# Optimization experiments

Measured on AMD Instinct MI355X. Metric: run time of the kernel, lower is better.

Reference implementation:

```python
import jax, jax.numpy as jnp
import numpy as np


def relu_bt(x):
    # -threshold(-leaky_relu(x), -t, -t) == min(leaky_relu(x), t), t = ||x||_inf (detached)
    t = jax.lax.stop_gradient(jnp.max(jnp.abs(x)))
    return jnp.minimum(jax.nn.leaky_relu(x, negative_slope=0.01), t)


def setup_inputs() -> dict:
    key = jax.random.key(0)
    k1, k2, k3, k4 = jax.random.split(key, 4)
    N, E, F_in, F_out = 100000, 1600000, 128, 64
    x = jax.random.normal(k1, (N, F_in), dtype=jnp.float32)
    edge_index = jax.random.randint(k2, (2, E), 0, N, dtype=jnp.int64)
    # xavier_normal with gain=1.414
    W = jax.random.normal(k3, (F_in, F_out), dtype=jnp.float32) * (1.414 * np.sqrt(2.0 / (F_in + F_out)))
    a = jax.random.normal(k4, (1, 4 * F_out), dtype=jnp.float32) * (1.414 * np.sqrt(2.0 / (1 + 4 * F_out)))
    return {"x": x, "edge_index": edge_index, "W": W, "a": a}


def reference(x, edge_index, W, a):
    N = x.shape[0]
    F_out = W.shape[1]
    h = x @ W  # [N, F_out]
    src = edge_index[0]
    dst = edge_index[1]
    hs = h[src]  # [E, F_out]
    hd = h[dst]  # [E, F_out]
    agg = relu_bt(hs + hd)
    diff = relu_bt(hs - hd)
    # a @ cat([hs, hd, agg, diff], dim=1).T == sum of four per-edge dot products
    a0, a1, a2, a3 = jnp.split(a.reshape(4 * F_out), 4)
    score = hs @ a0 + hd @ a1 + agg @ a2 + diff @ a3  # [E]
    edge_e = jnp.exp(-relu_bt(score))  # [E]
    # spmm(A, ones): rowsum over outgoing edges (grouped by src)
    e_rowsum = jax.ops.segment_sum(edge_e, src, num_segments=N)  # [N]
    # spmm(A, h): weighted aggregation of neighbor (dst) features into src rows
    h_prime = jax.ops.segment_sum(edge_e[:, None] * hd, src, num_segments=N)  # [N, F_out]
    return h_prime / (e_rowsum[:, None] + 1e-16)
```

## Files before the change

### kernel.cpp

```cpp
#include <hip/hip_runtime.h>
#include <hip/hip_fp16.h>

#define F_IN 128
#define F_OUT 64
#define BIN_TILE 2048
#define BSHIFT 8
#define BNODES 256
#define BCAP 6144u

#define LK_A 0.505f
#define LK_B 0.495f

__device__ __forceinline__ float leaky(float v) {
    return fmaf(LK_B, fabsf(v), LK_A * v);
}

template <int CTRL>
__device__ __forceinline__ float dppadd(float v) {
    return v + __builtin_bit_cast(float,
        __builtin_amdgcn_update_dpp(0, __builtin_bit_cast(int, v), CTRL, 0xf, 0xf, true));
}

__device__ __forceinline__ float sum8(float v) {
    v = dppadd<0xB1>(v);
    v = dppadd<0x4E>(v);
    v = dppadd<0x141>(v);
    return v;
}

__device__ __forceinline__ float xslot_sum2(float v) {
    v = dppadd<0x128>(v);
    v += __shfl_xor(v, 16);
    return v;
}

__device__ __forceinline__ float wave_sum(float v) {
    v += __builtin_bit_cast(float, __builtin_amdgcn_update_dpp(0, __builtin_bit_cast(int, v), 0x111, 0xf, 0xf, true));
    v += __builtin_bit_cast(float, __builtin_amdgcn_update_dpp(0, __builtin_bit_cast(int, v), 0x112, 0xf, 0xf, true));
    v += __builtin_bit_cast(float, __builtin_amdgcn_update_dpp(0, __builtin_bit_cast(int, v), 0x114, 0xf, 0xe, true));
    v += __builtin_bit_cast(float, __builtin_amdgcn_update_dpp(0, __builtin_bit_cast(int, v), 0x118, 0xf, 0xc, true));
    v += __builtin_bit_cast(float, __builtin_amdgcn_update_dpp(0, __builtin_bit_cast(int, v), 0x142, 0xa, 0xf, true));
    v += __builtin_bit_cast(float, __builtin_amdgcn_update_dpp(0, __builtin_bit_cast(int, v), 0x143, 0xc, 0xf, true));
    return __builtin_bit_cast(float, __builtin_amdgcn_readlane(__builtin_bit_cast(int, v), 63));
}

__device__ __forceinline__ void cvt8(const uint4 u, float* g) {
    float2 f;
    f = __half22float2(__builtin_bit_cast(__half2, u.x)); g[0] = f.x; g[1] = f.y;
    f = __half22float2(__builtin_bit_cast(__half2, u.y)); g[2] = f.x; g[3] = f.y;
    f = __half22float2(__builtin_bit_cast(__half2, u.z)); g[4] = f.x; g[5] = f.y;
    f = __half22float2(__builtin_bit_cast(__half2, u.w)); g[6] = f.x; g[7] = f.y;
}

__global__ __launch_bounds__(256) void gemm_xw(const float* __restrict__ x,
                                               const float* __restrict__ W,
                                               float* __restrict__ h32,
                                               uint2* __restrict__ h16,
                                               unsigned* __restrict__ gcur,
                                               int N, int NB, unsigned cap, int mode) {
    if (gcur && blockIdx.x == 0)
        for (int i = threadIdx.x; i < NB; i += 256) gcur[i] = (unsigned)i * cap;

    __shared__ float w_lds[F_IN][F_OUT];
    {
        const float4* Wv = (const float4*)W;
        float4* wl = (float4*)w_lds;
        for (int i = threadIdx.x; i < F_IN * F_OUT / 4; i += 256) wl[i] = Wv[i];
    }
    __syncthreads();

    const int cg = threadIdx.x & 15;
    const int rs = threadIdx.x >> 4;
    const int row0 = blockIdx.x * 128 + rs * 8;

    int r[8];
#pragma unroll
    for (int i = 0; i < 8; ++i) { const int rr = row0 + i; r[i] = rr < N ? rr : N - 1; }

    float4 acc[8];
#pragma unroll
    for (int i = 0; i < 8; ++i) acc[i] = make_float4(0.f, 0.f, 0.f, 0.f);

    float4 xc[8];
#pragma unroll
    for (int i = 0; i < 8; ++i) xc[i] = *(const float4*)(x + (size_t)r[i] * F_IN);

    for (int k4 = 0; k4 < 32; ++k4) {
        float4 xn[8];
        if (k4 < 31) {
#pragma unroll
            for (int i = 0; i < 8; ++i)
                xn[i] = *(const float4*)(x + (size_t)r[i] * F_IN + (k4 + 1) * 4);
        }
        float4 wv[4];
#pragma unroll
        for (int kk = 0; kk < 4; ++kk)
            wv[kk] = *(const float4*)&w_lds[k4 * 4 + kk][cg * 4];

#pragma unroll
        for (int i = 0; i < 8; ++i) {
            acc[i].x = fmaf(xc[i].x, wv[0].x, acc[i].x);
            acc[i].y = fmaf(xc[i].x, wv[0].y, acc[i].y);
            acc[i].z = fmaf(xc[i].x, wv[0].z, acc[i].z);
            acc[i].w = fmaf(xc[i].x, wv[0].w, acc[i].w);
            acc[i].x = fmaf(xc[i].y, wv[1].x, acc[i].x);
            acc[i].y = fmaf(xc[i].y, wv[1].y, acc[i].y);
            acc[i].z = fmaf(xc[i].y, wv[1].z, acc[i].z);
            acc[i].w = fmaf(xc[i].y, wv[1].w, acc[i].w);
            acc[i].x = fmaf(xc[i].z, wv[2].x, acc[i].x);
            acc[i].y = fmaf(xc[i].z, wv[2].y, acc[i].y);
            acc[i].z = fmaf(xc[i].z, wv[2].z, acc[i].z);
            acc[i].w = fmaf(xc[i].z, wv[2].w, acc[i].w);
            acc[i].x = fmaf(xc[i].w, wv[3].x, acc[i].x);
            acc[i].y = fmaf(xc[i].w, wv[3].y, acc[i].y);
            acc[i].z = fmaf(xc[i].w, wv[3].z, acc[i].z);
            acc[i].w = fmaf(xc[i].w, wv[3].w, acc[i].w);
        }
        if (k4 < 31) {
#pragma unroll
            for (int i = 0; i < 8; ++i) xc[i] = xn[i];
        }
    }

#pragma unroll
    for (int i = 0; i < 8; ++i) {
        const int rr = row0 + i;
        if (rr < N) {
            if (mode & 2) *(float4*)(h32 + (size_t)rr * F_OUT + cg * 4) = acc[i];
            if (mode & 1) {
                uint2 u;
                u.x = __builtin_bit_cast(unsigned, __floats2half2_rn(acc[i].x, acc[i].y));
                u.y = __builtin_bit_cast(unsigned, __floats2half2_rn(acc[i].z, acc[i].w));
                h16[(size_t)rr * 16 + cg] = u;
            }
        }
    }
}

__global__ __launch_bounds__(256) void binA(const int* __restrict__ ei,
                                            unsigned* __restrict__ gcur,
                                            unsigned* __restrict__ binned,
                                            int E, int NB, unsigned cap) {
    __shared__ unsigned lcnt[1024];
    __shared__ unsigned lbase[1024];
    const int t = threadIdx.x;
    for (int i = t; i < NB; i += 256) lcnt[i] = 0;
    __syncthreads();
    const int base = blockIdx.x * BIN_TILE;
    unsigned pk[8], bk[8], rk[8];
#pragma unroll
    for (int i = 0; i < 8; ++i) {
        const int e = base + i * 256 + t;
        if (e < E) {
            const unsigned s = (unsigned)ei[e];
            const unsigned d = (unsigned)ei[E + e];
            bk[i] = s >> BSHIFT;
            pk[i] = ((s & (BNODES - 1u)) << 17) | d;
            rk[i] = atomicAdd(&lcnt[bk[i]], 1u);
        }
    }
    __syncthreads();
    for (int i = t; i < NB; i += 256) {
        const unsigned c = lcnt[i];
        lbase[i] = c ? atomicAdd(&gcur[i], c) : 0u;
    }
    __syncthreads();
#pragma unroll
    for (int i = 0; i < 8; ++i) {
        const int e = base + i * 256 + t;
        if (e < E) {
            const unsigned pos = lbase[bk[i]] + rk[i];
            if (pos < (bk[i] + 1u) * cap) binned[pos] = pk[i];
        }
    }
}

__global__ __launch_bounds__(256) void binB(const unsigned* __restrict__ binned,
                                            const unsigned* __restrict__ gcur,
                                            unsigned* __restrict__ off,
                                            unsigned* __restrict__ deg,
                                            int* __restrict__ sdst,
                                            int N, int NB, unsigned cap) {
    __shared__ unsigned stg[BCAP];
    __shared__ unsigned ncnt[BNODES];
    __shared__ unsigned ts[256];
    const int b = blockIdx.x;
    const int t = threadIdx.x;
    const unsigned src0 = (unsigned)b * cap;
    unsigned sz = gcur[b] - src0; if (sz > cap) sz = cap;

    ncnt[t] = 0;
    for (unsigned i = t; i < sz; i += 256) stg[i] = binned[src0 + i];
    __syncthreads();

    for (unsigned i = t; i < sz; i += 256) atomicAdd(&ncnt[stg[i] >> 17], 1u);
    __syncthreads();

    const unsigned myc = ncnt[t];
    ts[t] = myc;
    __syncthreads();
    for (int st = 1; st < 256; st <<= 1) {
        const unsigned add = (t >= st) ? ts[t - st] : 0u;
        __syncthreads();
        ts[t] += add;
        __syncthreads();
    }
    const unsigned excl = ts[t] - myc;
    ncnt[t] = excl;
    const int g = (b << BSHIFT) + t;
    if (g < N) { off[g] = src0 + excl; deg[g] = myc; }
    __syncthreads();

    for (unsigned i = t; i < sz; i += 256) {
        const unsigned p = stg[i];
        const unsigned pos = atomicAdd(&ncnt[p >> 17], 1u);
        sdst[src0 + pos] = (int)(p & 0x1FFFFu);
    }
}

__global__ __launch_bounds__(256) void node_kernel(const unsigned* __restrict__ off,
                                                   const unsigned* __restrict__ deg,
                                                   const int* __restrict__ sdst,
                                                   const uint2* __restrict__ h16v,
                                                   const float* __restrict__ a,
                                                   float* __restrict__ out, int N) {
    const int lane  = threadIdx.x & 63;
    const int half  = lane >> 5;
    const int slot4 = (lane >> 3) & 3;
    const int q     = lane & 7;
    const char* h16 = (const char*)h16v;

    float b1[8], a2b[8], a3b[8], a0m[8];
#pragma unroll
    for (int f = 0; f < 8; ++f) {
        const float A0 = a[q * 8 + f];
        const float A1 = a[64 + q * 8 + f];
        const float A2 = a[128 + q * 8 + f];
        const float A3 = a[192 + q * 8 + f];
        b1[f]  = fmaf(LK_A, A2 - A3, A1);
        a2b[f] = LK_B * A2;
        a3b[f] = LK_B * A3;
        a0m[f] = fmaf(LK_A, A2 + A3, A0);
    }

    const int wid = (int)((blockIdx.x * 256u + threadIdx.x) >> 6);
    const int nw  = (int)((gridDim.x * 256u) >> 6);

    int pr = wid;
    if (pr * 2 >= N) return;

    int node = pr * 2 + half;
    int nc = (node < N) ? node : N - 1;
    unsigned bg  = off[nc];
    unsigned dgv = (node < N) ? deg[nc] : 0u;
    uint4 hsu = *(const uint4*)(h16 + ((size_t)nc << 7) + q * 16);
    int dA0 = 0;
    {
        const int len0 = (int)dgv;
        if (len0 > 0) { int e0 = slot4; const int lm = len0 - 1; if (e0 > lm) e0 = lm; dA0 = sdst[bg + e0]; }
    }

    while (true) {
        const int prn = pr + nw;
        const bool hasNext = (prn * 2 < N);

        const int len = (int)dgv;
        const unsigned beg = bg;
        float hs[8]; cvt8(hsu, hs);

        int noden = 0, ncn = 0; unsigned bgn = 0, dgn = 0;
        uint4 hsun = make_uint4(0u, 0u, 0u, 0u);
        if (hasNext) {
            noden = prn * 2 + half;
            ncn = (noden < N) ? noden : N - 1;
            bgn = off[ncn];
            dgn = (noden < N) ? deg[ncn] : 0u;
            hsun = *(const uint4*)(h16 + ((size_t)ncn << 7) + q * 16);
        }

        float csp = 0.f;
#pragma unroll
        for (int f = 0; f < 8; ++f) csp = fmaf(hs[f], a0m[f], csp);
        const float cs = sum8(csp);

        const int lenO = __shfl_xor(len, 32);
        const int ml = (len > lenO) ? len : lenO;

        float acc[8];
#pragma unroll
        for (int f = 0; f < 8; ++f) acc[f] = 0.f;
        float rsum = 0.f;

        const int lm1 = (len > 0) ? len - 1 : 0;
        uint4 uA = *(const uint4*)(h16 + ((size_t)dA0 << 7) + q * 16);
        int dB = dA0;
        if (len > 4) { int e1 = 4 + slot4; if (e1 > lm1) e1 = lm1; dB = sdst[beg + e1]; }
        uint4 uB = *(const uint4*)(h16 + ((size_t)dB << 7) + q * 16);
        int dC = dB;
        if (len > 8) { int e2 = 8 + slot4; if (e2 > lm1) e2 = lm1; dC = sdst[beg + e2]; }

        for (int cb = 0; cb < ml; cb += 4) {
            uint4 uC = uB;
            int dD = dC;
            if (cb + 8 < len)
                uC = *(const uint4*)(h16 + ((size_t)dC << 7) + q * 16);
            if (cb + 12 < len) { int e3 = cb + 12 + slot4; if (e3 > lm1) e3 = lm1; dD = sdst[beg + e3]; }

            float g[8];
            cvt8(uA, g);
            float p0 = 0.f, p1 = 0.f;
#pragma unroll
            for (int f = 0; f < 8; f += 2) {
                const float sa0 = hs[f] + g[f],         sb0 = hs[f] - g[f];
                const float sa1 = hs[f + 1] + g[f + 1], sb1 = hs[f + 1] - g[f + 1];
                p0 = fmaf(g[f],     b1[f],     p0);
                p1 = fmaf(g[f + 1], b1[f + 1], p1);
                p0 = fmaf(fabsf(sa0), a2b[f],     p0);
                p1 = fmaf(fabsf(sa1), a2b[f + 1], p1);
                p0 = fmaf(fabsf(sb0), a3b[f],     p0);
                p1 = fmaf(fabsf(sb1), a3b[f + 1], p1);
            }
            const float R = sum8(p0 + p1);

            float e = __expf(-leaky(cs + R));
            e = (cb + slot4 < len) ? e : 0.f;
#pragma unroll
            for (int f = 0; f < 8; ++f) acc[f] = fmaf(e, g[f], acc[f]);
            rsum += e;

            uA = uB; uB = uC; dC = dD;
        }

        int dA0n = 0;
        if (hasNext) {
            const int lenn = (int)dgn;
            if (lenn > 0) { int e0 = slot4; const int lm = lenn - 1; if (e0 > lm) e0 = lm; dA0n = sdst[bgn + e0]; }
        }

#pragma unroll
        for (int f = 0; f < 8; ++f) acc[f] = xslot_sum2(acc[f]);
        rsum = xslot_sum2(rsum);

        if (slot4 == 0 && node < N) {
            const float inv = 1.f / (rsum + 1e-16f);
            float4 o0, o1;
            o0.x = acc[0] * inv; o0.y = acc[1] * inv; o0.z = acc[2] * inv; o0.w = acc[3] * inv;
            o1.x = acc[4] * inv; o1.y = acc[5] * inv; o1.z = acc[6] * inv; o1.w = acc[7] * inv;
            float* orow = out + (size_t)node * F_OUT + q * 8;
            *(float4*)orow = o0;
            *(float4*)(orow + 4) = o1;
        }

        if (!hasNext) break;
        pr = prn; node = noden; nc = ncn; bg = bgn; dgv = dgn; hsu = hsun; dA0 = dA0n;
    }
}

__global__ __launch_bounds__(256) void hist_kernel(const int* __restrict__ ei,
                                                   unsigned* __restrict__ cnt, int E) {
    const int e = blockIdx.x * 256 + threadIdx.x;
    if (e < E) atomicAdd(&cnt[ei[e]], 1u);
}

__global__ __launch_bounds__(256) void scan1(const unsigned* __restrict__ cnt,
                                             unsigned* __restrict__ bsum, int n) {
    __shared__ unsigned lds[256];
    const int t = threadIdx.x;
    const int base = blockIdx.x * 2048 + t * 8;
    unsigned s = 0;
#pragma unroll
    for (int i = 0; i < 8; ++i) { const int idx = base + i; if (idx < n) s += cnt[idx]; }
    lds[t] = s; __syncthreads();
    for (int st = 128; st > 0; st >>= 1) {
        if (t < st) lds[t] += lds[t + st];
        __syncthreads();
    }
    if (t == 0) bsum[blockIdx.x] = lds[0];
}

__global__ __launch_bounds__(128) void scan2(unsigned* __restrict__ bsum,
                                             unsigned* __restrict__ off, int nb, int n) {
    __shared__ unsigned lds[128];
    const int t = threadIdx.x;
    if (t < nb) lds[t] = bsum[t];
    __syncthreads();
    if (t == 0) {
        unsigned run = 0;
        for (int i = 0; i < nb; ++i) { const unsigned v = lds[i]; lds[i] = run; run += v; }
        off[n] = run;
    }
    __syncthreads();
    if (t < nb) bsum[t] = lds[t];
}

__global__ __launch_bounds__(256) void scan3(const unsigned* __restrict__ cnt,
                                             const unsigned* __restrict__ bsum,
                                             unsigned* __restrict__ off,
                                             unsigned* __restrict__ cursor, int n) {
    __shared__ unsigned lds[256];
    const int t = threadIdx.x;
    const int base = blockIdx.x * 2048 + t * 8;
    unsigned v[8]; unsigned s = 0;
#pragma unroll
    for (int i = 0; i < 8; ++i) { const int idx = base + i; v[i] = (idx < n) ? cnt[idx] : 0u; s += v[i]; }
    lds[t] = s; __syncthreads();
    for (int st = 1; st < 256; st <<= 1) {
        const unsigned add = (t >= st) ? lds[t - st] : 0u;
        __syncthreads();
        lds[t] += add;
        __syncthreads();
    }
    unsigned excl = (t > 0 ? lds[t - 1] : 0u) + bsum[blockIdx.x];
#pragma unroll
    for (int i = 0; i < 8; ++i) {
        const int idx = base + i;
        if (idx < n) { off[idx] = excl; cursor[idx] = excl; excl += v[i]; }
    }
}

__global__ __launch_bounds__(256) void scatter_kernel(const int* __restrict__ ei,
                                                      unsigned* __restrict__ cursor,
                                                      int* __restrict__ sdst, int E) {
    const int e = blockIdx.x * 256 + threadIdx.x;
    if (e >= E) return;
    const int s = ei[e];
    const int d = ei[E + e];
    const unsigned pos = atomicAdd(&cursor[s], 1u);
    sdst[pos] = d;
}

__device__ __forceinline__ float edge_part(float hs, float hd, float a1, float a2, float a3) {
    float p = hd * a1;
    p = fmaf(leaky(hs + hd), a2, p);
    p = fmaf(leaky(hs - hd), a3, p);
    return p;
}

__global__ __launch_bounds__(256) void edge_kernel(const int* __restrict__ ei,
                                                   const float* __restrict__ h,
                                                   const float* __restrict__ a,
                                                   float* __restrict__ hprime,
                                                   float* __restrict__ rowsum,
                                                   int E) {
    const int lane = threadIdx.x & 63;
    const int wave = (int)((blockIdx.x * blockDim.x + threadIdx.x) >> 6);
    const int nwaves = (int)((gridDim.x * blockDim.x) >> 6);
    const float a0 = a[lane], a1 = a[64 + lane], a2 = a[128 + lane], a3 = a[192 + lane];
    for (int e = wave; e < E; e += nwaves) {
        const int s = ei[e];
        const int d = ei[E + e];
        const float hs = h[(size_t)s * F_OUT + lane];
        const float hd = h[(size_t)d * F_OUT + lane];
        const float part = wave_sum(hs * a0 + edge_part(hs, hd, a1, a2, a3));
        const float ee = __expf(-leaky(part));
        atomicAdd(&hprime[(size_t)s * F_OUT + lane], ee * hd);
        if (lane == 0) atomicAdd(&rowsum[s], ee);
    }
}

__global__ __launch_bounds__(256) void finalize(float* __restrict__ out,
                                                const float* __restrict__ rowsum,
                                                int total) {
    const int i = blockIdx.x * blockDim.x + threadIdx.x;
    if (i < total) out[i] = out[i] / (rowsum[i >> 6] + 1e-16f);
}

static inline size_t align_up(size_t v, size_t a) { return (v + a - 1) & ~(a - 1); }

extern "C" void kernel_launch(void* const* d_in, const int* in_sizes, int n_in,
                              void* d_out, int out_size, void* d_ws, size_t ws_size,
                              hipStream_t stream) {
    const float* x  = (const float*)d_in[0];
    const int*   ei = (const int*)d_in[1];
    const float* W  = (const float*)d_in[2];
    const float* a  = (const float*)d_in[3];

    const int N = in_sizes[0] / F_IN;
    const int E = in_sizes[1] / 2;
    float* out = (float*)d_out;

    const int NB = (N + BNODES - 1) >> BSHIFT;
    const int ngemm = (N + 127) / 128;
    const int nbt = (E + BIN_TILE - 1) / BIN_TILE;
    const unsigned meanFill = (NB > 0) ? (unsigned)(E / NB) : 0u;

    char* ws = (char*)d_ws;
    const size_t szh16  = align_up((size_t)N * F_OUT * 2, 256);
    const size_t szoff  = align_up(((size_t)N + 1) * 4, 256);
    const size_t szedge = align_up((size_t)E * 4 + 64, 256);
    const size_t szbin  = align_up((size_t)NB * BCAP * 4 + 64, 256);

    const size_t off_b  = szh16;
    const size_t deg_b    = off_b + szoff;
    const size_t sdstA_b  = deg_b + szoff;
    const size_t binned_b = sdstA_b + szbin;
    const size_t gcur_b   = binned_b + szbin;
    const size_t needA    = gcur_b + 4096;
    const size_t sdstB_b  = off_b + szoff;
    const size_t cursor_b = sdstB_b + szedge;
    const size_t cnt_b    = cursor_b + align_up((size_t)N * 4, 256);
    const size_t bsum_b   = cnt_b + align_up((size_t)N * 4, 256);
    const size_t needB    = bsum_b + 4096;

    uint2* h16 = (uint2*)ws;
    const int nodeBlocks = 2048;

    if (ws_size >= needA && N <= (1 << 17) && NB <= 1024 && meanFill <= (BCAP * 3u) / 4u) {
        unsigned* off    = (unsigned*)(ws + off_b);
        unsigned* deg    = (unsigned*)(ws + deg_b);
        int*      sdst   = (int*)(ws + sdstA_b);
        unsigned* binned = (unsigned*)(ws + binned_b);
        unsigned* gcur   = (unsigned*)(ws + gcur_b);

        gemm_xw<<<ngemm, 256, 0, stream>>>(x, W, nullptr, h16, gcur, N, NB, BCAP, 1);
        binA<<<nbt, 256, 0, stream>>>(ei, gcur, binned, E, NB, BCAP);
        binB<<<NB, 256, 0, stream>>>(binned, gcur, off, deg, sdst, N, NB, BCAP);
        node_kernel<<<nodeBlocks, 256, 0, stream>>>(off, deg, sdst, h16, a, out, N);
    } else if (ws_size >= needB && N <= (1 << 17)) {
        unsigned* off    = (unsigned*)(ws + off_b);
        int*      sdst   = (int*)(ws + sdstB_b);
        unsigned* cursor = (unsigned*)(ws + cursor_b);
        unsigned* cnt    = (unsigned*)(ws + cnt_b);
        unsigned* bsum   = (unsigned*)(ws + bsum_b);
        const int nb2 = (N + 2047) / 2048;

        hipMemsetAsync(cnt, 0, (size_t)N * 4, stream);
        gemm_xw<<<ngemm, 256, 0, stream>>>(x, W, nullptr, h16, nullptr, N, NB, BCAP, 1);
        hist_kernel<<<(E + 255) / 256, 256, 0, stream>>>(ei, cnt, E);
        scan1<<<nb2, 256, 0, stream>>>(cnt, bsum, N);
        scan2<<<1, 128, 0, stream>>>(bsum, off, nb2, N);
        scan3<<<nb2, 256, 0, stream>>>(cnt, bsum, off, cursor, N);
        scatter_kernel<<<(E + 255) / 256, 256, 0, stream>>>(ei, cursor, sdst, E);
        node_kernel<<<nodeBlocks, 256, 0, stream>>>(off, cnt, sdst, h16, a, out, N);
    } else {
        float* h32    = (float*)ws;
        float* rowsum = (float*)(ws + align_up((size_t)N * F_OUT * 4, 256));
        hipMemsetAsync(d_out, 0, (size_t)N * F_OUT * sizeof(float), stream);
        hipMemsetAsync(rowsum, 0, (size_t)N * sizeof(float), stream);
        gemm_xw<<<ngemm, 256, 0, stream>>>(x, W, h32, nullptr, nullptr, N, NB, BCAP, 2);
        edge_kernel<<<2048, 256, 0, stream>>>(ei, h32, a, out, rowsum, E);
        finalize<<<((size_t)N * F_OUT + 255) / 256, 256, 0, stream>>>(out, rowsum, N * F_OUT);
    }
}
```

Baseline: 147.5 us.

## Fuse GEMM with edge binning and merge bucket sort into per-bucket node kernel

Merges the x@W GEMM and the first edge-binning pass into one launch, with blocks split by index so the two jobs run concurrently. Bins shrink to 64 nodes each, and a new bucket_node kernel does the per-node counting sort in LDS and then computes attention and aggregation straight from the staged edges. It also stages source-node features in LDS, which removes the separate binB pass and its global sdst/off/deg round trip. The cost is more, smaller bins with fixed capacity, so overflow risk rises when degree is skewed, and node work per block is tied to bucket size.

New measurement: 131.4 us. 1.12x faster.

```diff
diff --git a/kernel.cpp b/kernel.cpp
--- a/kernel.cpp
+++ b/kernel.cpp
@@ -4,9 +4,9 @@
 #define F_IN 128
 #define F_OUT 64
 #define BIN_TILE 2048
-#define BSHIFT 8
-#define BNODES 256
-#define BCAP 6144u
+#define BSHIFT 6
+#define BNODES 64
+#define BCAP 2048u
 
 #define LK_A 0.505f
 #define LK_B 0.495f
@@ -52,170 +52,354 @@
     f = __half22float2(__builtin_bit_cast(__half2, u.w)); g[6] = f.x; g[7] = f.y;
 }
 
-__global__ __launch_bounds__(256) void gemm_xw(const float* __restrict__ x,
-                                               const float* __restrict__ W,
-                                               float* __restrict__ h32,
-                                               uint2* __restrict__ h16,
-                                               unsigned* __restrict__ gcur,
-                                               int N, int NB, unsigned cap, int mode) {
-    if (gcur && blockIdx.x == 0)
-        for (int i = threadIdx.x; i < NB; i += 256) gcur[i] = (unsigned)i * cap;
-
-    __shared__ float w_lds[F_IN][F_OUT];
-    {
-        const float4* Wv = (const float4*)W;
-        float4* wl = (float4*)w_lds;
-        for (int i = threadIdx.x; i < F_IN * F_OUT / 4; i += 256) wl[i] = Wv[i];
-    }
-    __syncthreads();
-
-    const int cg = threadIdx.x & 15;
-    const int rs = threadIdx.x >> 4;
-    const int row0 = blockIdx.x * 128 + rs * 8;
-
-    int r[8];
-#pragma unroll
-    for (int i = 0; i < 8; ++i) { const int rr = row0 + i; r[i] = rr < N ? rr : N - 1; }
-
-    float4 acc[8];
-#pragma unroll
-    for (int i = 0; i < 8; ++i) acc[i] = make_float4(0.f, 0.f, 0.f, 0.f);
-
-    float4 xc[8];
-#pragma unroll
-    for (int i = 0; i < 8; ++i) xc[i] = *(const float4*)(x + (size_t)r[i] * F_IN);
-
-    for (int k4 = 0; k4 < 32; ++k4) {
-        float4 xn[8];
-        if (k4 < 31) {
-#pragma unroll
-            for (int i = 0; i < 8; ++i)
-                xn[i] = *(const float4*)(x + (size_t)r[i] * F_IN + (k4 + 1) * 4);
-        }
-        float4 wv[4];
-#pragma unroll
-        for (int kk = 0; kk < 4; ++kk)
-            wv[kk] = *(const float4*)&w_lds[k4 * 4 + kk][cg * 4];
+__global__ __launch_bounds__(256) void gemm_binA(const float* __restrict__ x,
+                                                 const float* __restrict__ W,
+                                                 float* __restrict__ h32,
+                                                 uint2* __restrict__ h16,
+                                                 const int* __restrict__ ei,
+                                                 unsigned* __restrict__ gcur,
+                                                 unsigned* __restrict__ binned,
+                                                 int N, int E, int NB, int ngemm,
+                                                 unsigned cap, int mode) {
+    __shared__ unsigned smem_u[8192];
+
+    if ((int)blockIdx.x < ngemm) {
+        float (*w_lds)[F_OUT] = (float (*)[F_OUT])smem_u;
+        {
+            const float4* Wv = (const float4*)W;
+            float4* wl = (float4*)w_lds;
+            for (int i = threadIdx.x; i < F_IN * F_OUT / 4; i += 256) wl[i] = Wv[i];
+        }
+        __syncthreads();
+
+        const int cg = threadIdx.x & 15;
+        const int rs = threadIdx.x >> 4;
+        const int row0 = blockIdx.x * 128 + rs * 8;
+
+        int r[8];
+#pragma unroll
+        for (int i = 0; i < 8; ++i) { const int rr = row0 + i; r[i] = rr < N ? rr : N - 1; }
+
+        float4 acc[8];
+#pragma unroll
+        for (int i = 0; i < 8; ++i) acc[i] = make_float4(0.f, 0.f, 0.f, 0.f);
+
+        float4 xc[8];
+#pragma unroll
+        for (int i = 0; i < 8; ++i) xc[i] = *(const float4*)(x + (size_t)r[i] * F_IN);
+
+        for (int k4 = 0; k4 < 32; ++k4) {
+            float4 xn[8];
+            if (k4 < 31) {
+#pragma unroll
+                for (int i = 0; i < 8; ++i)
+                    xn[i] = *(const float4*)(x + (size_t)r[i] * F_IN + (k4 + 1) * 4);
+            }
+            float4 wv[4];
+#pragma unroll
+            for (int kk = 0; kk < 4; ++kk)
+                wv[kk] = *(const float4*)&w_lds[k4 * 4 + kk][cg * 4];
+
+#pragma unroll
+            for (int i = 0; i < 8; ++i) {
+                acc[i].x = fmaf(xc[i].x, wv[0].x, acc[i].x);
+                acc[i].y = fmaf(xc[i].x, wv[0].y, acc[i].y);
+                acc[i].z = fmaf(xc[i].x, wv[0].z, acc[i].z);
+                acc[i].w = fmaf(xc[i].x, wv[0].w, acc[i].w);
+                acc[i].x = fmaf(xc[i].y, wv[1].x, acc[i].x);
+                acc[i].y = fmaf(xc[i].y, wv[1].y, acc[i].y);
+                acc[i].z = fmaf(xc[i].y, wv[1].z, acc[i].z);
+                acc[i].w = fmaf(xc[i].y, wv[1].w, acc[i].w);
+                acc[i].x = fmaf(xc[i].z, wv[2].x, acc[i].x);
+                acc[i].y = fmaf(xc[i].z, wv[2].y, acc[i].y);
+                acc[i].z = fmaf(xc[i].z, wv[2].z, acc[i].z);
+                acc[i].w = fmaf(xc[i].z, wv[2].w, acc[i].w);
+                acc[i].x = fmaf(xc[i].w, wv[3].x, acc[i].x);
+                acc[i].y = fmaf(xc[i].w, wv[3].y, acc[i].y);
+                acc[i].z = fmaf(xc[i].w, wv[3].z, acc[i].z);
+                acc[i].w = fmaf(xc[i].w, wv[3].w, acc[i].w);
+            }
+            if (k4 < 31) {
+#pragma unroll
+                for (int i = 0; i < 8; ++i) xc[i] = xn[i];
+            }
+        }
 
 #pragma unroll
         for (int i = 0; i < 8; ++i) {
-            acc[i].x = fmaf(xc[i].x, wv[0].x, acc[i].x);
-            acc[i].y = fmaf(xc[i].x, wv[0].y, acc[i].y);
-            acc[i].z = fmaf(xc[i].x, wv[0].z, acc[i].z);
-            acc[i].w = fmaf(xc[i].x, wv[0].w, acc[i].w);
-            acc[i].x = fmaf(xc[i].y, wv[1].x, acc[i].x);
-            acc[i].y = fmaf(xc[i].y, wv[1].y, acc[i].y);
-            acc[i].z = fmaf(xc[i].y, wv[1].z, acc[i].z);
-            acc[i].w = fmaf(xc[i].y, wv[1].w, acc[i].w);
-            acc[i].x = fmaf(xc[i].z, wv[2].x, acc[i].x);
-            acc[i].y = fmaf(xc[i].z, wv[2].y, acc[i].y);
-            acc[i].z = fmaf(xc[i].z, wv[2].z, acc[i].z);
-            acc[i].w = fmaf(xc[i].z, wv[2].w, acc[i].w);
-            acc[i].x = fmaf(xc[i].w, wv[3].x, acc[i].x);
-            acc[i].y = fmaf(xc[i].w, wv[3].y, acc[i].y);
-            acc[i].z = fmaf(xc[i].w, wv[3].z, acc[i].z);
-            acc[i].w = fmaf(xc[i].w, wv[3].w, acc[i].w);
-        }
-        if (k4 < 31) {
-#pragma unroll
-            for (int i = 0; i < 8; ++i) xc[i] = xn[i];
-        }
-    }
-
-#pragma unroll
-    for (int i = 0; i < 8; ++i) {
-        const int rr = row0 + i;
-        if (rr < N) {
-            if (mode & 2) *(float4*)(h32 + (size_t)rr * F_OUT + cg * 4) = acc[i];
-            if (mode & 1) {
-                uint2 u;
-                u.x = __builtin_bit_cast(unsigned, __floats2half2_rn(acc[i].x, acc[i].y));
-                u.y = __builtin_bit_cast(unsigned, __floats2half2_rn(acc[i].z, acc[i].w));
-                h16[(size_t)rr * 16 + cg] = u;
-            }
-        }
-    }
-}
-
-__global__ __launch_bounds__(256) void binA(const int* __restrict__ ei,
-                                            unsigned* __restrict__ gcur,
-                                            unsigned* __restrict__ binned,
-                                            int E, int NB, unsigned cap) {
-    __shared__ unsigned lcnt[1024];
-    __shared__ unsigned lbase[1024];
-    const int t = threadIdx.x;
-    for (int i = t; i < NB; i += 256) lcnt[i] = 0;
-    __syncthreads();
-    const int base = blockIdx.x * BIN_TILE;
-    unsigned pk[8], bk[8], rk[8];
-#pragma unroll
-    for (int i = 0; i < 8; ++i) {
-        const int e = base + i * 256 + t;
-        if (e < E) {
-            const unsigned s = (unsigned)ei[e];
-            const unsigned d = (unsigned)ei[E + e];
-            bk[i] = s >> BSHIFT;
-            pk[i] = ((s & (BNODES - 1u)) << 17) | d;
-            rk[i] = atomicAdd(&lcnt[bk[i]], 1u);
-        }
-    }
-    __syncthreads();
-    for (int i = t; i < NB; i += 256) {
-        const unsigned c = lcnt[i];
-        lbase[i] = c ? atomicAdd(&gcur[i], c) : 0u;
-    }
-    __syncthreads();
-#pragma unroll
-    for (int i = 0; i < 8; ++i) {
-        const int e = base + i * 256 + t;
-        if (e < E) {
-            const unsigned pos = lbase[bk[i]] + rk[i];
-            if (pos < (bk[i] + 1u) * cap) binned[pos] = pk[i];
-        }
-    }
-}
-
-__global__ __launch_bounds__(256) void binB(const unsigned* __restrict__ binned,
-                                            const unsigned* __restrict__ gcur,
-                                            unsigned* __restrict__ off,
-                                            unsigned* __restrict__ deg,
-                                            int* __restrict__ sdst,
-                                            int N, int NB, unsigned cap) {
+            const int rr = row0 + i;
+            if (rr < N) {
+                if (mode & 2) *(float4*)(h32 + (size_t)rr * F_OUT + cg * 4) = acc[i];
+                if (mode & 1) {
+                    uint2 u;
+                    u.x = __builtin_bit_cast(unsigned, __floats2half2_rn(acc[i].x, acc[i].y));
+                    u.y = __builtin_bit_cast(unsigned, __floats2half2_rn(acc[i].z, acc[i].w));
+                    h16[(size_t)rr * 16 + cg] = u;
+                }
+            }
+        }
+    } else {
+        unsigned* lcnt  = smem_u;
+        unsigned* lbase = smem_u + 2048;
+        const int t = threadIdx.x;
+        for (int i = t; i < NB; i += 256) lcnt[i] = 0;
+        __syncthreads();
+        const int base = ((int)blockIdx.x - ngemm) * BIN_TILE;
+        unsigned pk[8], bk[8], rk[8];
+#pragma unroll
+        for (int i = 0; i < 8; ++i) {
+            const int e = base + i * 256 + t;
+            if (e < E) {
+                const unsigned s = (unsigned)ei[e];
+                const unsigned d = (unsigned)ei[E + e];
+                bk[i] = s >> BSHIFT;
+                pk[i] = ((s & (BNODES - 1u)) << 17) | d;
+                rk[i] = atomicAdd(&lcnt[bk[i]], 1u);
+            }
+        }
+        __syncthreads();
+        for (int i = t; i < NB; i += 256) {
+            const unsigned c = lcnt[i];
+            lbase[i] = c ? atomicAdd(&gcur[i], c) : 0u;
+        }
+        __syncthreads();
+#pragma unroll
+        for (int i = 0; i < 8; ++i) {
+            const int e = base + i * 256 + t;
+            if (e < E) {
+                const unsigned po = lbase[bk[i]] + rk[i];
+                if (po < cap) binned[(size_t)bk[i] * cap + po] = pk[i];
+            }
+        }
+    }
+}
+
+__global__ __launch_bounds__(256) void bucket_node(const unsigned* __restrict__ binned,
+                                                   const unsigned* __restrict__ gcur,
+                                                   const uint2* __restrict__ h16v,
+                                                   const float* __restrict__ a,
+                                                   float* __restrict__ out,
+                                                   int N, unsigned cap) {
     __shared__ unsigned stg[BCAP];
-    __shared__ unsigned ncnt[BNODES];
-    __shared__ unsigned ts[256];
+    __shared__ uint4    hsl[BNODES * 8];
+    __shared__ unsigned ndeg[BNODES];
+    __shared__ unsigned nbase[BNODES];
+    __shared__ unsigned ncur[BNODES];
+    __shared__ unsigned ts[BNODES];
+
     const int b = blockIdx.x;
     const int t = threadIdx.x;
-    const unsigned src0 = (unsigned)b * cap;
-    unsigned sz = gcur[b] - src0; if (sz > cap) sz = cap;
-
-    ncnt[t] = 0;
-    for (unsigned i = t; i < sz; i += 256) stg[i] = binned[src0 + i];
+    const int node0 = b << BSHIFT;
+    const size_t src0 = (size_t)b * cap;
+    unsigned sz = gcur[b]; if (sz > cap) sz = cap;
+
+    if (t < BNODES) ndeg[t] = 0;
+    {
+        const uint4* hsrc = (const uint4*)h16v;
+        const int limit = N * 8;
+#pragma unroll
+        for (int k = 0; k < (BNODES * 8) / 256; ++k) {
+            const int i = k * 256 + t;
+            const int gi = node0 * 8 + i;
+            hsl[i] = (gi < limit) ? hsrc[gi] : make_uint4(0u, 0u, 0u, 0u);
+        }
+    }
     __syncthreads();
 
-    for (unsigned i = t; i < sz; i += 256) atomicAdd(&ncnt[stg[i] >> 17], 1u);
+    for (unsigned i = t; i < sz; i += 256)
+        atomicAdd(&ndeg[binned[src0 + i] >> 17], 1u);
     __syncthreads();
 
-    const unsigned myc = ncnt[t];
-    ts[t] = myc;
+    if (t < BNODES) ts[t] = ndeg[t];
     __syncthreads();
+    for (int st = 1; st < BNODES; st <<= 1) {
+        unsigned add = 0;
+        if (t < BNODES && t >= st) add = ts[t - st];
+        __syncthreads();
+        if (t < BNODES) ts[t] += add;
+        __syncthreads();
+    }
+    if (t < BNODES) {
+        const unsigned ex = ts[t] - ndeg[t];
+        nbase[t] = ex;
+        ncur[t]  = ex;
+    }
+    __syncthreads();
+
+    for (unsigned i = t; i < sz; i += 256) {
+        const unsigned p = binned[src0 + i];
+        const unsigned pos = atomicAdd(&ncur[p >> 17], 1u);
+        stg[pos] = p & 0x1FFFFu;
+    }
+    __syncthreads();
+
+    const int lane  = t & 63;
+    const int half  = lane >> 5;
+    const int slot4 = (lane >> 3) & 3;
+    const int q     = lane & 7;
+    const int slot8 = (t >> 6) * 2 + half;
+    const char* h16 = (const char*)h16v;
+
+    float b1[8], a2b[8], a3b[8], a0m[8];
+#pragma unroll
+    for (int f = 0; f < 8; ++f) {
+        const float A0 = a[q * 8 + f];
+        const float A1 = a[64 + q * 8 + f];
+        const float A2 = a[128 + q * 8 + f];
+        const float A3 = a[192 + q * 8 + f];
+        b1[f]  = fmaf(LK_A, A2 - A3, A1);
+        a2b[f] = LK_B * A2;
+        a3b[f] = LK_B * A3;
+        a0m[f] = fmaf(LK_A, A2 + A3, A0);
+    }
+
+#pragma unroll 1
+    for (int nn = 0; nn < BNODES / 8; ++nn) {
+        const int nloc = slot8 * (BNODES / 8) + nn;
+        const int node = node0 + nloc;
+        const int beg = (int)nbase[nloc];
+        const int len = (int)ndeg[nloc];
+
+        float hs[8]; cvt8(hsl[nloc * 8 + q], hs);
+        float csp = 0.f;
+#pragma unroll
+        for (int f = 0; f < 8; ++f) csp = fmaf(hs[f], a0m[f], csp);
+        const float cs = sum8(csp);
+
+        float acc[8];
+#pragma unroll
+        for (int f = 0; f < 8; ++f) acc[f] = 0.f;
+        float rsum = 0.f;
+
+        const int lm1 = (len > 0) ? len - 1 : 0;
+        int dA = 0;
+        if (len > 0) { int e0 = slot4; if (e0 > lm1) e0 = lm1; dA = (int)stg[beg + e0]; }
+        uint4 uA = *(const uint4*)(h16 + ((size_t)dA << 7) + q * 16);
+        int dB = dA;
+        if (len > 4) { int e1 = 4 + slot4; if (e1 > lm1) e1 = lm1; dB = (int)stg[beg + e1]; }
+        uint4 uB = *(const uint4*)(h16 + ((size_t)dB << 7) + q * 16);
+        int dC = dB;
+        if (len > 8) { int e2 = 8 + slot4; if (e2 > lm1) e2 = lm1; dC = (int)stg[beg + e2]; }
+
+        for (int cb = 0; cb < len; cb += 4) {
+            uint4 uC = uB;
+            int dD = dC;
+            if (cb + 8 < len)
+                uC = *(const uint4*)(h16 + ((size_t)dC << 7) + q * 16);
+            if (cb + 12 < len) { int e3 = cb + 12 + slot4; if (e3 > lm1) e3 = lm1; dD = (int)stg[beg + e3]; }
+
+            float g[8];
+            cvt8(uA, g);
+            float p0 = 0.f, p1 = 0.f;
+#pragma unroll
+            for (int f = 0; f < 8; f += 2) {
+                const float sa0 = hs[f] + g[f],         sb0 = hs[f] - g[f];
+                const float sa1 = hs[f + 1] + g[f + 1], sb1 = hs[f + 1] - g[f + 1];
+                p0 = fmaf(g[f],     b1[f],     p0);
+                p1 = fmaf(g[f + 1], b1[f + 1], p1);
+                p0 = fmaf(fabsf(sa0), a2b[f],     p0);
+                p1 = fmaf(fabsf(sa1), a2b[f + 1], p1);
+                p0 = fmaf(fabsf(sb0), a3b[f],     p0);
+                p1 = fmaf(fabsf(sb1), a3b[f + 1], p1);
+            }
+            const float R = sum8(p0 + p1);
+
+            float e = __expf(-leaky(cs + R));
+            e = (cb + slot4 < len) ? e : 0.f;
+#pragma unroll
+            for (int f = 0; f < 8; ++f) acc[f] = fmaf(e, g[f], acc[f]);
+            rsum += e;
+
+            uA = uB; uB = uC; dC = dD;
+        }
+
+#pragma unroll
+        for (int f = 0; f < 8; ++f) acc[f] = xslot_sum2(acc[f]);
+        rsum = xslot_sum2(rsum);
+
+        if (slot4 == 0 && node < N) {
+            const float inv = 1.f / (rsum + 1e-16f);
+            float4 o0, o1;
+            o0.x = acc[0] * inv; o0.y = acc[1] * inv; o0.z = acc[2] * inv; o0.w = acc[3] * inv;
+            o1.x = acc[4] * inv; o1.y = acc[5] * inv; o1.z = acc[6] * inv; o1.w = acc[7] * inv;
+            float* orow = out + (size_t)node * F_OUT + q * 8;
+            *(float4*)orow = o0;
+            *(float4*)(orow + 4) = o1;
+        }
+    }
+}
+
+__global__ __launch_bounds__(256) void hist_kernel(const int* __restrict__ ei,
+                                                   unsigned* __restrict__ cnt, int E) {
+    const int e = blockIdx.x * 256 + threadIdx.x;
+    if (e < E) atomicAdd(&cnt[ei[e]], 1u);
+}
+
+__global__ __launch_bounds__(256) void scan1(const unsigned* __restrict__ cnt,
+                                             unsigned* __restrict__ bsum, int n) {
+    __shared__ unsigned lds[256];
+    const int t = threadIdx.x;
+    const int base = blockIdx.x * 2048 + t * 8;
+    unsigned s = 0;
+#pragma unroll
+    for (int i = 0; i < 8; ++i) { const int idx = base + i; if (idx < n) s += cnt[idx]; }
+    lds[t] = s; __syncthreads();
+    for (int st = 128; st > 0; st >>= 1) {
+        if (t < st) lds[t] += lds[t + st];
+        __syncthreads();
+    }
+    if (t == 0) bsum[blockIdx.x] = lds[0];
+}
+
+__global__ __launch_bounds__(128) void scan2(unsigned* __restrict__ bsum,
+                                             unsigned* __restrict__ off, int nb, int n) {
+    __shared__ unsigned lds[128];
+    const int t = threadIdx.x;
+    if (t < nb) lds[t] = bsum[t];
+    __syncthreads();
+    if (t == 0) {
+        unsigned run = 0;
+        for (int i = 0; i < nb; ++i) { const unsigned v = lds[i]; lds[i] = run; run += v; }
+        off[n] = run;
+    }
+    __syncthreads();
+    if (t < nb) bsum[t] = lds[t];
+}
+
+__global__ __launch_bounds__(256) void scan3(const unsigned* __restrict__ cnt,
+                                             const unsigned* __restrict__ bsum,
+                                             unsigned* __restrict__ off,
+                                             unsigned* __restrict__ cursor, int n) {
+    __shared__ unsigned lds[256];
+    const int t = threadIdx.x;
+    const int base = blockIdx.x * 2048 + t * 8;
+    unsigned v[8]; unsigned s = 0;
+#pragma unroll
+    for (int i = 0; i < 8; ++i) { const int idx = base + i; v[i] = (idx < n) ? cnt[idx] : 0u; s += v[i]; }
+    lds[t] = s; __syncthreads();
     for (int st = 1; st < 256; st <<= 1) {
-        const unsigned add = (t >= st) ? ts[t - st] : 0u;
-        __syncthreads();
-        ts[t] += add;
-        __syncthreads();
-    }
-    const unsigned excl = ts[t] - myc;
-    ncnt[t] = excl;
-    const int g = (b << BSHIFT) + t;
-    if (g < N) { off[g] = src0 + excl; deg[g] = myc; }
-    __syncthreads();
-
-    for (unsigned i = t; i < sz; i += 256) {
-        const unsigned p = stg[i];
-        const unsigned pos = atomicAdd(&ncnt[p >> 17], 1u);
-        sdst[src0 + pos] = (int)(p & 0x1FFFFu);
-    }
+        const unsigned add = (t >= st) ? lds[t - st] : 0u;
+        __syncthreads();
+        lds[t] += add;
+        __syncthreads();
+    }
+    unsigned excl = (t > 0 ? lds[t - 1] : 0u) + bsum[blockIdx.x];
+#pragma unroll
+    for (int i = 0; i < 8; ++i) {
+        const int idx = base + i;
+        if (idx < n) { off[idx] = excl; cursor[idx] = excl; excl += v[i]; }
+    }
+}
+
+__global__ __launch_bounds__(256) void scatter_kernel(const int* __restrict__ ei,
+                                                      unsigned* __restrict__ cursor,
+                                                      int* __restrict__ sdst, int E) {
+    const int e = blockIdx.x * 256 + threadIdx.x;
+    if (e >= E) return;
+    const int s = ei[e];
+    const int d = ei[E + e];
+    const unsigned pos = atomicAdd(&cursor[s], 1u);
+    sdst[pos] = d;
 }
 
 __global__ __launch_bounds__(256) void node_kernel(const unsigned* __restrict__ off,
@@ -246,38 +430,14 @@
     const int wid = (int)((blockIdx.x * 256u + threadIdx.x) >> 6);
     const int nw  = (int)((gridDim.x * 256u) >> 6);
 
-    int pr = wid;
-    if (pr * 2 >= N) return;
-
-    int node = pr * 2 + half;
-    int nc = (node < N) ? node : N - 1;
-    unsigned bg  = off[nc];
-    unsigned dgv = (node < N) ? deg[nc] : 0u;
-    uint4 hsu = *(const uint4*)(h16 + ((size_t)nc << 7) + q * 16);
-    int dA0 = 0;
-    {
-        const int len0 = (int)dgv;
-        if (len0 > 0) { int e0 = slot4; const int lm = len0 - 1; if (e0 > lm) e0 = lm; dA0 = sdst[bg + e0]; }
-    }
-
-    while (true) {
-        const int prn = pr + nw;
-        const bool hasNext = (prn * 2 < N);
-
-        const int len = (int)dgv;
-        const unsigned beg = bg;
-        float hs[8]; cvt8(hsu, hs);
-
-        int noden = 0, ncn = 0; unsigned bgn = 0, dgn = 0;
-        uint4 hsun = make_uint4(0u, 0u, 0u, 0u);
-        if (hasNext) {
-            noden = prn * 2 + half;
-            ncn = (noden < N) ? noden : N - 1;
-            bgn = off[ncn];
-            dgn = (noden < N) ? deg[ncn] : 0u;
-            hsun = *(const uint4*)(h16 + ((size_t)ncn << 7) + q * 16);
-        }
-
+    for (int pr = wid; pr * 2 < N; pr += nw) {
+        const int node = pr * 2 + half;
+        const int nc = (node < N) ? node : N - 1;
+        const unsigned beg = off[nc];
+        const int len = (node < N) ? (int)deg[nc] : 0;
+
+        float hs[8];
+        cvt8(*(const uint4*)(h16 + ((size_t)nc << 7) + q * 16), hs);
         float csp = 0.f;
 #pragma unroll
         for (int f = 0; f < 8; ++f) csp = fmaf(hs[f], a0m[f], csp);
@@ -292,8 +452,10 @@
         float rsum = 0.f;
 
         const int lm1 = (len > 0) ? len - 1 : 0;
-        uint4 uA = *(const uint4*)(h16 + ((size_t)dA0 << 7) + q * 16);
-        int dB = dA0;
+        int dA = 0;
+        if (len > 0) { int e0 = slot4; if (e0 > lm1) e0 = lm1; dA = sdst[beg + e0]; }
+        uint4 uA = *(const uint4*)(h16 + ((size_t)dA << 7) + q * 16);
+        int dB = dA;
         if (len > 4) { int e1 = 4 + slot4; if (e1 > lm1) e1 = lm1; dB = sdst[beg + e1]; }
         uint4 uB = *(const uint4*)(h16 + ((size_t)dB << 7) + q * 16);
         int dC = dB;
@@ -321,20 +483,12 @@
                 p1 = fmaf(fabsf(sb1), a3b[f + 1], p1);
             }
             const float R = sum8(p0 + p1);
-
             float e = __expf(-leaky(cs + R));
             e = (cb + slot4 < len) ? e : 0.f;
 #pragma unroll
             for (int f = 0; f < 8; ++f) acc[f] = fmaf(e, g[f], acc[f]);
             rsum += e;
-
             uA = uB; uB = uC; dC = dD;
-        }
-
-        int dA0n = 0;
-        if (hasNext) {
-            const int lenn = (int)dgn;
-            if (lenn > 0) { int e0 = slot4; const int lm = lenn - 1; if (e0 > lm) e0 = lm; dA0n = sdst[bgn + e0]; }
         }
 
 #pragma unroll
@@ -350,83 +504,7 @@
             *(float4*)orow = o0;
             *(float4*)(orow + 4) = o1;
         }
-
-        if (!hasNext) break;
-        pr = prn; node = noden; nc = ncn; bg = bgn; dgv = dgn; hsu = hsun; dA0 = dA0n;
-    }
-}
-
-__global__ __launch_bounds__(256) void hist_kernel(const int* __restrict__ ei,
-                                                   unsigned* __restrict__ cnt, int E) {
-    const int e = blockIdx.x * 256 + threadIdx.x;
-    if (e < E) atomicAdd(&cnt[ei[e]], 1u);
-}
-
-__global__ __launch_bounds__(256) void scan1(const unsigned* __restrict__ cnt,
-                                             unsigned* __restrict__ bsum, int n) {
-    __shared__ unsigned lds[256];
-    const int t = threadIdx.x;
-    const int base = blockIdx.x * 2048 + t * 8;
-    unsigned s = 0;
-#pragma unroll
-    for (int i = 0; i < 8; ++i) { const int idx = base + i; if (idx < n) s += cnt[idx]; }
-    lds[t] = s; __syncthreads();
-    for (int st = 128; st > 0; st >>= 1) {
-        if (t < st) lds[t] += lds[t + st];
-        __syncthreads();
-    }
-    if (t == 0) bsum[blockIdx.x] = lds[0];
-}
-
-__global__ __launch_bounds__(128) void scan2(unsigned* __restrict__ bsum,
-                                             unsigned* __restrict__ off, int nb, int n) {
-    __shared__ unsigned lds[128];
-    const int t = threadIdx.x;
-    if (t < nb) lds[t] = bsum[t];
-    __syncthreads();
-    if (t == 0) {
-        unsigned run = 0;
-        for (int i = 0; i < nb; ++i) { const unsigned v = lds[i]; lds[i] = run; run += v; }
-        off[n] = run;
-    }
-    __syncthreads();
-    if (t < nb) bsum[t] = lds[t];
-}
-
-__global__ __launch_bounds__(256) void scan3(const unsigned* __restrict__ cnt,
-                                             const unsigned* __restrict__ bsum,
-                                             unsigned* __restrict__ off,
-                                             unsigned* __restrict__ cursor, int n) {
-    __shared__ unsigned lds[256];
-    const int t = threadIdx.x;
-    const int base = blockIdx.x * 2048 + t * 8;
-    unsigned v[8]; unsigned s = 0;
-#pragma unroll
-    for (int i = 0; i < 8; ++i) { const int idx = base + i; v[i] = (idx < n) ? cnt[idx] : 0u; s += v[i]; }
-    lds[t] = s; __syncthreads();
-    for (int st = 1; st < 256; st <<= 1) {
-        const unsigned add = (t >= st) ? lds[t - st] : 0u;
-        __syncthreads();
-        lds[t] += add;
-        __syncthreads();
-    }
-    unsigned excl = (t > 0 ? lds[t - 1] : 0u) + bsum[blockIdx.x];
-#pragma unroll
-    for (int i = 0; i < 8; ++i) {
-        const int idx = base + i;
-        if (idx < n) { off[idx] = excl; cursor[idx] = excl; excl += v[i]; }
-    }
-}
-
-__global__ __launch_bounds__(256) void scatter_kernel(const int* __restrict__ ei,
-                                                      unsigned* __restrict__ cursor,
-                                                      int* __restrict__ sdst, int E) {
-    const int e = blockIdx.x * 256 + threadIdx.x;
-    if (e >= E) return;
-    const int s = ei[e];
-    const int d = ei[E + e];
-    const unsigned pos = atomicAdd(&cursor[s], 1u);
-    sdst[pos] = d;
+    }
 }
 
 __device__ __forceinline__ float edge_part(float hs, float hd, float a1, float a2, float a3) {
@@ -490,54 +568,50 @@
     const size_t szedge = align_up((size_t)E * 4 + 64, 256);
     const size_t szbin  = align_up((size_t)NB * BCAP * 4 + 64, 256);
 
-    const size_t off_b  = szh16;
-    const size_t deg_b    = off_b + szoff;
-    const size_t sdstA_b  = deg_b + szoff;
-    const size_t binned_b = sdstA_b + szbin;
-    const size_t gcur_b   = binned_b + szbin;
-    const size_t needA    = gcur_b + 4096;
-    const size_t sdstB_b  = off_b + szoff;
+    const size_t binned_b = szh16;
+    const size_t gcurA_b  = binned_b + szbin;
+    const size_t needA    = gcurA_b + align_up((size_t)NB * 4, 256);
+    const size_t offB_b   = szh16;
+    const size_t degB_b   = offB_b + szoff;
+    const size_t sdstB_b  = degB_b + szoff;
     const size_t cursor_b = sdstB_b + szedge;
-    const size_t cnt_b    = cursor_b + align_up((size_t)N * 4, 256);
-    const size_t bsum_b   = cnt_b + align_up((size_t)N * 4, 256);
+    const size_t bsum_b   = cursor_b + align_up((size_t)N * 4, 256);
     const size_t needB    = bsum_b + 4096;
 
     uint2* h16 = (uint2*)ws;
-    const int nodeBlocks = 2048;
-
-    if (ws_size >= needA && N <= (1 << 17) && NB <= 1024 && meanFill <= (BCAP * 3u) / 4u) {
-        unsigned* off    = (unsigned*)(ws + off_b);
-        unsigned* deg    = (unsigned*)(ws + deg_b);
-        int*      sdst   = (int*)(ws + sdstA_b);
+
+    if (ws_size >= needA && N <= (1 << 17) && NB <= 2048 && meanFill <= (BCAP * 3u) / 4u) {
         unsigned* binned = (unsigned*)(ws + binned_b);
-        unsigned* gcur   = (unsigned*)(ws + gcur_b);
-
-        gemm_xw<<<ngemm, 256, 0, stream>>>(x, W, nullptr, h16, gcur, N, NB, BCAP, 1);
-        binA<<<nbt, 256, 0, stream>>>(ei, gcur, binned, E, NB, BCAP);
-        binB<<<NB, 256, 0, stream>>>(binned, gcur, off, deg, sdst, N, NB, BCAP);
-        node_kernel<<<nodeBlocks, 256, 0, stream>>>(off, deg, sdst, h16, a, out, N);
+        unsigned* gcur   = (unsigned*)(ws + gcurA_b);
+
+        hipMemsetAsync(gcur, 0, (size_t)NB * 4, stream);
+        gemm_binA<<<ngemm + nbt, 256, 0, stream>>>(x, W, nullptr, h16, ei, gcur, binned,
+                                                   N, E, NB, ngemm, BCAP, 1);
+        bucket_node<<<NB, 256, 0, stream>>>(binned, gcur, h16, a, out, N, BCAP);
     } else if (ws_size >= needB && N <= (1 << 17)) {
-        unsigned* off    = (unsigned*)(ws + off_b);
+        unsigned* off    = (unsigned*)(ws + offB_b);
+        unsigned* deg    = (unsigned*)(ws + degB_b);
         int*      sdst   = (int*)(ws + sdstB_b);
         unsigned* cursor = (unsigned*)(ws + cursor_b);
-        unsigned* cnt    = (unsigned*)(ws + cnt_b);
         unsigned* bsum   = (unsigned*)(ws + bsum_b);
         const int nb2 = (N + 2047) / 2048;
 
-        hipMemsetAsync(cnt, 0, (size_t)N * 4, stream);
-        gemm_xw<<<ngemm, 256, 0, stream>>>(x, W, nullptr, h16, nullptr, N, NB, BCAP, 1);
-        hist_kernel<<<(E + 255) / 256, 256, 0, stream>>>(ei, cnt, E);
-        scan1<<<nb2, 256, 0, stream>>>(cnt, bsum, N);
+        hipMemsetAsync(deg, 0, (size_t)N * 4, stream);
+        gemm_binA<<<ngemm, 256, 0, stream>>>(x, W, nullptr, h16, ei, nullptr, nullptr,
+                                             N, E, NB, ngemm, BCAP, 1);
+        hist_kernel<<<(E + 255) / 256, 256, 0, stream>>>(ei, deg, E);
+        scan1<<<nb2, 256, 0, stream>>>(deg, bsum, N);
         scan2<<<1, 128, 0, stream>>>(bsum, off, nb2, N);
-        scan3<<<nb2, 256, 0, stream>>>(cnt, bsum, off, cursor, N);
+        scan3<<<nb2, 256, 0, stream>>>(deg, bsum, off, cursor, N);
         scatter_kernel<<<(E + 255) / 256, 256, 0, stream>>>(ei, cursor, sdst, E);
-        node_kernel<<<nodeBlocks, 256, 0, stream>>>(off, cnt, sdst, h16, a, out, N);
+        node_kernel<<<2048, 256, 0, stream>>>(off, deg, sdst, h16, a, out, N);
     } else {
         float* h32    = (float*)ws;
         float* rowsum = (float*)(ws + align_up((size_t)N * F_OUT * 4, 256));
         hipMemsetAsync(d_out, 0, (size_t)N * F_OUT * sizeof(float), stream);
         hipMemsetAsync(rowsum, 0, (size_t)N * sizeof(float), stream);
-        gemm_xw<<<ngemm, 256, 0, stream>>>(x, W, h32, nullptr, nullptr, N, NB, BCAP, 2);
+        gemm_binA<<<ngemm, 256, 0, stream>>>(x, W, h32, nullptr, ei, nullptr, nullptr,
+                                             N, E, NB, ngemm, BCAP, 2);
         edge_kernel<<<2048, 256, 0, stream>>>(ei, h32, a, out, rowsum, E);
         finalize<<<((size_t)N * F_OUT + 255) / 256, 256, 0, stream>>>(out, rowsum, N * F_OUT);
     }
```
